# Performance work log

Hardware: AMD Instinct MI355X
Metric: run time of the kernel (lower is better)

Reference implementation:

```python
import jax, jax.numpy as jnp
import numpy as np

B, S, D, H = 2, 2048, 2048, 16
DH = D // H  # 128 head dim
ROPE_THETA = 10000.0
LN_EPS = 1e-5


def setup_inputs() -> dict:
    key = jax.random.key(0)
    k1, k2, k3 = jax.random.split(key, 3)
    positions = jnp.broadcast_to(jnp.arange(S, dtype=jnp.int64), (B, S))
    hidden_states = jax.random.normal(k1, (B, S, D), dtype=jnp.float32)
    w_qkv = jax.random.normal(k2, (D, 3 * D), dtype=jnp.float32) * 0.02
    w_out = jax.random.normal(k3, (D, D), dtype=jnp.float32) * 0.02
    return {"positions": positions, "hidden_states": hidden_states,
            "w_qkv": w_qkv, "w_out": w_out}


def _rope(x, positions):
    # NeoX-style rotary (vLLM get_rope default): rotate split halves.
    # x: [B, S, H, DH], positions: [B, S]
    half = DH // 2
    inv_freq = 1.0 / (ROPE_THETA ** (jnp.arange(0, half, dtype=jnp.float32) / half))
    ang = positions.astype(jnp.float32)[..., None] * inv_freq  # [B, S, half]
    cos = jnp.cos(ang)[:, :, None, :]  # [B, S, 1, half]
    sin = jnp.sin(ang)[:, :, None, :]
    x1, x2 = x[..., :half], x[..., half:]
    return jnp.concatenate([x1 * cos - x2 * sin, x2 * cos + x1 * sin], axis=-1)


def reference(positions, hidden_states, w_qkv, w_out):
    # LayerNorm with no affine params (elementwise_affine=False)
    mu = jnp.mean(hidden_states, axis=-1, keepdims=True)
    var = jnp.mean(jnp.square(hidden_states - mu), axis=-1, keepdims=True)
    x = (hidden_states - mu) * jax.lax.rsqrt(var + LN_EPS)

    qkv = jnp.einsum('bsd,de->bse', x, w_qkv)  # [B, S, 3D]
    q, k, v = jnp.split(qkv, 3, axis=-1)
    q = q.reshape(B, S, H, DH)
    k = k.reshape(B, S, H, DH)
    v = v.reshape(B, S, H, DH)

    q = _rope(q, positions)
    k = _rope(k, positions)

    scale = DH ** -0.5
    scores = jnp.einsum('bqhd,bkhd->bhqk', q, k) * scale  # [B, H, S, S]
    causal = jnp.tril(jnp.ones((S, S), dtype=bool))
    scores = jnp.where(causal, scores, jnp.finfo(scores.dtype).min)
    probs = jax.nn.softmax(scores, axis=-1)
    attn = jnp.einsum('bhqk,bkhd->bqhd', probs, v).reshape(B, S, D)

    return jnp.einsum('bsd,de->bse', attn, w_out)
```

## Files before the change

### kernel.cpp

```cpp
#include <hip/hip_runtime.h>


typedef __bf16 bf16x8 __attribute__((ext_vector_type(8)));
typedef float f32x4 __attribute__((ext_vector_type(4)));
typedef unsigned short u16x8 __attribute__((ext_vector_type(8)));

__device__ __forceinline__ unsigned short f2bf(float f) {
  unsigned u = __builtin_bit_cast(unsigned, f);
  u = u + 0x7fffu + ((u >> 16) & 1u);
  return (unsigned short)(u >> 16);
}

#define GLD_LDS16(gp, lp)                                                      \
  __builtin_amdgcn_global_load_lds((__attribute__((address_space(1))) void*)(gp), \
                                   (__attribute__((address_space(3))) void*)(lp), \
                                   16, 0, 0)

__global__ __launch_bounds__(256) void prep_kernel(const float* __restrict__ hs,
                                                   const float* __restrict__ wqkv,
                                                   const float* __restrict__ wout,
                                                   unsigned short* __restrict__ xb,
                                                   unsigned short* __restrict__ wqkvT,
                                                   unsigned short* __restrict__ woutT) {
  const int tid = threadIdx.x;
  int bx = blockIdx.x;
  if (bx < 4096) {
    const float* rp = hs + (size_t)bx * 2048;
    const float4 v0 = ((const float4*)rp)[tid];
    const float4 v1 = ((const float4*)rp)[tid + 256];
    float s  = v0.x + v0.y + v0.z + v0.w + v1.x + v1.y + v1.z + v1.w;
    float ss = v0.x*v0.x + v0.y*v0.y + v0.z*v0.z + v0.w*v0.w
             + v1.x*v1.x + v1.y*v1.y + v1.z*v1.z + v1.w*v1.w;
#pragma unroll
    for (int m = 1; m < 64; m <<= 1) { s += __shfl_xor(s, m); ss += __shfl_xor(ss, m); }
    __shared__ float rs[4], rss[4];
    if ((tid & 63) == 0) { rs[tid >> 6] = s; rss[tid >> 6] = ss; }
    __syncthreads();
    s  = rs[0] + rs[1] + rs[2] + rs[3];
    ss = rss[0] + rss[1] + rss[2] + rss[3];
    const float mean = s * (1.0f / 2048.0f);
    const float var  = ss * (1.0f / 2048.0f) - mean * mean;
    const float inv  = rsqrtf(var + 1e-5f);
    ushort4 o0, o1;
    o0.x = f2bf((v0.x - mean) * inv); o0.y = f2bf((v0.y - mean) * inv);
    o0.z = f2bf((v0.z - mean) * inv); o0.w = f2bf((v0.w - mean) * inv);
    o1.x = f2bf((v1.x - mean) * inv); o1.y = f2bf((v1.y - mean) * inv);
    o1.z = f2bf((v1.z - mean) * inv); o1.w = f2bf((v1.w - mean) * inv);
    ushort4* op = (ushort4*)(xb + (size_t)bx * 2048);
    op[tid] = o0; op[tid + 256] = o1;
    return;
  }
  bx -= 4096;
  const float* in;
  unsigned short* out;
  int N, nt, kt;
  if (bx < 3072) { in = wqkv; out = wqkvT; N = 6144; nt = bx % 96; kt = bx / 96; }
  else { bx -= 3072; in = wout; out = woutT; N = 2048; nt = bx & 31; kt = bx >> 5; }
  const int n0 = nt * 64, k0 = kt * 64;
  __shared__ float t[64 * 65];
  const int tx4 = (tid & 15) * 4, ty = tid >> 4;
#pragma unroll
  for (int i = 0; i < 4; i++) {
    const int k = ty + i * 16;
    const float4 v = *(const float4*)&in[(size_t)(k0 + k) * N + n0 + tx4];
    t[(tx4 + 0) * 65 + k] = v.x;
    t[(tx4 + 1) * 65 + k] = v.y;
    t[(tx4 + 2) * 65 + k] = v.z;
    t[(tx4 + 3) * 65 + k] = v.w;
  }
  __syncthreads();
  const int kc = (tid & 7) * 8, nr = tid >> 3;
#pragma unroll
  for (int i = 0; i < 2; i++) {
    const int n = nr + i * 32;
    u16x8 o;
#pragma unroll
    for (int j = 0; j < 8; j++) o[j] = f2bf(t[n * 65 + kc + j]);
    *(u16x8*)&out[(size_t)(n0 + n) * 2048 + k0 + kc] = o;
  }
}

template <int OUT_BF16, int K>
__global__ __launch_bounds__(256) void gemm_bt(const unsigned short* __restrict__ A,
                                               const unsigned short* __restrict__ Bt,
                                               void* __restrict__ Cv,
                                               int M, int N) {
  __shared__ alignas(16) unsigned short sA[128 * 64];
  __shared__ alignas(16) unsigned short sB[128 * 64];
  const int tid = threadIdx.x;
  const int lane = tid & 63, wave = tid >> 6;
  const int wm = wave >> 1, wn = wave & 1;
  const int ln15 = lane & 15, quad = lane >> 4;
  const size_t m0 = (size_t)blockIdx.y * 128, n0 = (size_t)blockIdx.x * 128;
  const unsigned short* Ag = A + m0 * (size_t)K;
  const unsigned short* Bg = Bt + n0 * (size_t)K;
  const int lr8 = lane >> 3;
  const int sc8 = ((lane & 7) ^ (lr8 & 7)) * 8;
  const int xk = ln15 & 7;

  const unsigned short* pA[4];
  const unsigned short* pB[4];
#pragma unroll
  for (int i = 0; i < 4; i++) {
    const int row = (wave * 4 + i) * 8 + lr8;
    pA[i] = Ag + (size_t)row * K + sc8;
    pB[i] = Bg + (size_t)row * K + sc8;
  }

  f32x4 acc[4][4];
#pragma unroll
  for (int mi = 0; mi < 4; mi++)
#pragma unroll
    for (int ni = 0; ni < 4; ni++) acc[mi][ni] = (f32x4){0.f, 0.f, 0.f, 0.f};

#define K_STEP(U)                                                              \
  {                                                                            \
    __syncthreads();                                                           \
    _Pragma("unroll") for (int i = 0; i < 4; i++) {                            \
      GLD_LDS16(pA[i] + (U) * 64, &sA[(wave * 4 + i) * 512]);                  \
      GLD_LDS16(pB[i] + (U) * 64, &sB[(wave * 4 + i) * 512]);                  \
    }                                                                          \
    __syncthreads();                                                           \
    _Pragma("unroll") for (int ks = 0; ks < 2; ks++) {                         \
      bf16x8 af[4], bf[4];                                                     \
      _Pragma("unroll") for (int mi = 0; mi < 4; mi++)                         \
        af[mi] = *(const bf16x8*)&sA[(wm * 64 + mi * 16 + ln15) * 64 +         \
                                     ((ks * 4 + quad) ^ xk) * 8];              \
      _Pragma("unroll") for (int ni = 0; ni < 4; ni++)                         \
        bf[ni] = *(const bf16x8*)&sB[(wn * 64 + ni * 16 + ln15) * 64 +         \
                                     ((ks * 4 + quad) ^ xk) * 8];              \
      _Pragma("unroll") for (int mi = 0; mi < 4; mi++)                         \
        _Pragma("unroll") for (int ni = 0; ni < 4; ni++)                       \
          acc[mi][ni] = __builtin_amdgcn_mfma_f32_16x16x32_bf16(               \
              af[mi], bf[ni], acc[mi][ni], 0, 0, 0);                           \
    }                                                                          \
  }

#pragma unroll 1
  for (int kt4 = 0; kt4 < K / 256; ++kt4) {
    K_STEP(0) K_STEP(1) K_STEP(2) K_STEP(3)
#pragma unroll
    for (int i = 0; i < 4; i++) { pA[i] += 256; pB[i] += 256; }
  }
#undef K_STEP

#pragma unroll
  for (int mi = 0; mi < 4; mi++)
#pragma unroll
    for (int ni = 0; ni < 4; ni++) {
      const size_t col = n0 + wn * 64 + ni * 16 + ln15;
#pragma unroll
      for (int r = 0; r < 4; r++) {
        const size_t row = m0 + wm * 64 + mi * 16 + quad * 4 + r;
        if (OUT_BF16)
          ((unsigned short*)Cv)[row * N + col] = f2bf(acc[mi][ni][r]);
        else
          ((float*)Cv)[row * N + col] = acc[mi][ni][r];
      }
    }
}

__global__ __launch_bounds__(256) void rv_kernel(const unsigned short* __restrict__ qkv,
                                                 unsigned short* __restrict__ Qo,
                                                 unsigned short* __restrict__ Ko,
                                                 unsigned short* __restrict__ VT) {
  const int tid = threadIdx.x;
  const int bx = blockIdx.x;
  if (bx < 2048) {
    const int t = bx * 256 + tid;
    const int g = t & 7;
    const int h = (t >> 3) & 15;
    const int row = t >> 7;
    const int s = row & 2047;
    const size_t base = (size_t)row * 6144 + h * 128 + g * 8;
    const bf16x8 q1 = *(const bf16x8*)&qkv[base];
    const bf16x8 q2 = *(const bf16x8*)&qkv[base + 64];
    const bf16x8 k1 = *(const bf16x8*)&qkv[base + 2048];
    const bf16x8 k2 = *(const bf16x8*)&qkv[base + 2048 + 64];
    const float qscale = 0.08838834764831845f;
    bf16x8 oq1, oq2, ok1, ok2;
#pragma unroll
    for (int j = 0; j < 8; j++) {
      const int i = g * 8 + j;
      const float freq = exp2f(-(float)i * (13.287712379549449f / 64.0f));
      float rev = (float)s * freq * 0.15915494309189535f;
      rev -= floorf(rev);
      const float ar = rev * 6.283185307179586f;
      const float sn = __sinf(ar), cs = __cosf(ar);
      const float a1 = (float)q1[j], a2 = (float)q2[j];
      const float b1 = (float)k1[j], b2 = (float)k2[j];
      oq1[j] = (__bf16)((a1 * cs - a2 * sn) * qscale);
      oq2[j] = (__bf16)((a2 * cs + a1 * sn) * qscale);
      ok1[j] = (__bf16)(b1 * cs - b2 * sn);
      ok2[j] = (__bf16)(b2 * cs + b1 * sn);
    }
    const size_t ob = ((size_t)(((row >> 11) << 4) + h) * 2048 + s) * 128 + g * 8;
    *(bf16x8*)&Qo[ob]      = oq1;
    *(bf16x8*)&Qo[ob + 64] = oq2;
    *(bf16x8*)&Ko[ob]      = ok1;
    *(bf16x8*)&Ko[ob + 64] = ok2;
    return;
  }
  const int idx = bx - 2048;
  const int s0 = (idx & 31) * 64;
  const int d0 = ((idx >> 5) & 1) * 64;
  const int bh = idx >> 6, b = bh >> 4, h = bh & 15;
  __shared__ unsigned short t[64 * 65];
  const int tx8 = (tid & 7) * 8, ty = tid >> 3;
#pragma unroll
  for (int i = 0; i < 2; i++) {
    const int s = ty + i * 32;
    const u16x8 v = *(const u16x8*)&qkv[(size_t)(b * 2048 + s0 + s) * 6144 +
                                        4096 + h * 128 + d0 + tx8];
#pragma unroll
    for (int j = 0; j < 8; j++) t[(tx8 + j) * 65 + s] = v[j];
  }
  __syncthreads();
  const int sc8 = (tid & 7) * 8, dr = tid >> 3;
#pragma unroll
  for (int i = 0; i < 2; i++) {
    const int d = dr + i * 32;
    u16x8 o;
#pragma unroll
    for (int j = 0; j < 8; j++) o[j] = t[d * 65 + sc8 + j];
    *(u16x8*)&VT[((size_t)bh * 128 + d0 + d) * 2048 + s0 + sc8] = o;
  }
}

__global__ __launch_bounds__(256) void flash_kernel(const unsigned short* __restrict__ Q,
                                                    const unsigned short* __restrict__ Kbuf,
                                                    const unsigned short* __restrict__ VT,
                                                    unsigned short* __restrict__ attn) {
  __shared__ alignas(16) unsigned short sK[2][64 * 128];
  __shared__ alignas(16) unsigned short sVT[2][128 * 64];
  __shared__ alignas(16) unsigned short sP[64 * 72];

  const int bh = blockIdx.y;
  const int b = bh >> 4, h = bh & 15;
  const int tid = threadIdx.x;
  const int lane = tid & 63, w = tid >> 6;
  const int ln15 = lane & 15, quad = lane >> 4;

  const unsigned short* Qg = Q + (size_t)bh * 2048 * 128;
  const unsigned short* Kg = Kbuf + (size_t)bh * 2048 * 128;
  const unsigned short* Vg = VT + (size_t)bh * 128 * 2048;

  const float L2E = 1.44269504088896f;
  bf16x8 onesf;
#pragma unroll
  for (int j = 0; j < 8; j++) onesf[j] = (__bf16)1.0f;

  const int kcrow = (lane >> 4);
  const int kch = (lane & 15);
  const int vcrow = (lane >> 3);
  const int vch = (lane & 7);
  const unsigned short* pK0[4];
  const unsigned short* pV0[4];
#pragma unroll
  for (int i = 0; i < 4; i++) {
    const int c = w * 4 + i;
    const int rowK = c * 4 + kcrow;
    pK0[i] = Kg + (size_t)rowK * 128 + (kch ^ (rowK & 15)) * 8;
    const int rowV = c * 8 + vcrow;
    pV0[i] = Vg + (size_t)rowV * 2048 + (vch ^ (rowV & 7)) * 8;
  }

#pragma unroll 1
  for (int t = 0; t < 2; t++) {
    const int qt = t ? (31 - (int)blockIdx.x) : (int)blockIdx.x;
    const int q0 = qt * 64;

    bf16x8 qf[4];
#pragma unroll
    for (int ks = 0; ks < 4; ks++)
      qf[ks] = *(const bf16x8*)&Qg[(size_t)(q0 + w * 16 + ln15) * 128 + ks * 32 + quad * 8];

    f32x4 o[8], ol;
#pragma unroll
    for (int nd = 0; nd < 8; nd++) o[nd] = (f32x4){0.f, 0.f, 0.f, 0.f};
    ol = (f32x4){0.f, 0.f, 0.f, 0.f};
    float mrow[4];
#pragma unroll
    for (int r = 0; r < 4; r++) mrow[r] = -1e30f;

    __syncthreads();
#pragma unroll
    for (int i = 0; i < 4; i++) GLD_LDS16(pK0[i], &sK[0][(w * 4 + i) * 512]);
#pragma unroll
    for (int i = 0; i < 4; i++) GLD_LDS16(pV0[i], &sVT[0][(w * 4 + i) * 512]);

    const unsigned short* pKn[4];
    const unsigned short* pVn[4];
#pragma unroll
    for (int i = 0; i < 4; i++) { pKn[i] = pK0[i] + 8192; pVn[i] = pV0[i] + 64; }

#pragma unroll 1
    for (int j = 0; j <= qt; j++) {
      const int cur = j & 1;
      __syncthreads();
      if (j < qt) {
        const int nxt = cur ^ 1;
#pragma unroll
        for (int i = 0; i < 4; i++) GLD_LDS16(pKn[i], &sK[nxt][(w * 4 + i) * 512]);
#pragma unroll
        for (int i = 0; i < 4; i++) GLD_LDS16(pVn[i], &sVT[nxt][(w * 4 + i) * 512]);
      }
#pragma unroll
      for (int i = 0; i < 4; i++) { pKn[i] += 8192; pVn[i] += 64; }

      f32x4 sc[4];
#pragma unroll
      for (int ni = 0; ni < 4; ni++) sc[ni] = (f32x4){0.f, 0.f, 0.f, 0.f};
      __builtin_amdgcn_s_setprio(1);
#pragma unroll
      for (int ks = 0; ks < 4; ks++) {
        bf16x8 bk[4];
#pragma unroll
        for (int ni = 0; ni < 4; ni++) {
          const int row = ni * 16 + ln15;
          const int ch = (ks * 4 + quad) ^ (row & 15);
          bk[ni] = *(const bf16x8*)&sK[cur][row * 128 + ch * 8];
        }
#pragma unroll
        for (int ni = 0; ni < 4; ni++)
          sc[ni] = __builtin_amdgcn_mfma_f32_16x16x32_bf16(qf[ks], bk[ni], sc[ni], 0, 0, 0);
      }
      __builtin_amdgcn_s_setprio(0);

      float mt[4] = {-1e30f, -1e30f, -1e30f, -1e30f};
      if (j == qt) {
        const int k0 = j * 64;
#pragma unroll
        for (int ni = 0; ni < 4; ni++) {
          const int key = k0 + ni * 16 + ln15;
#pragma unroll
          for (int r = 0; r < 4; r++) {
            const int qrow = q0 + w * 16 + quad * 4 + r;
            float v = sc[ni][r];
            if (key > qrow) v = -1e30f;
            sc[ni][r] = v;
            mt[r] = fmaxf(mt[r], v);
          }
        }
      } else {
#pragma unroll
        for (int ni = 0; ni < 4; ni++)
#pragma unroll
          for (int r = 0; r < 4; r++) mt[r] = fmaxf(mt[r], sc[ni][r]);
      }
      float m4[4];
#pragma unroll
      for (int r = 0; r < 4; r++) {
        float m = mt[r];
        m = fmaxf(m, __shfl_xor(m, 1));
        m = fmaxf(m, __shfl_xor(m, 2));
        m = fmaxf(m, __shfl_xor(m, 4));
        m = fmaxf(m, __shfl_xor(m, 8));
        m4[r] = m;
      }
      const bool defer = (m4[0] <= mrow[0] + 8.0f) & (m4[1] <= mrow[1] + 8.0f) &
                         (m4[2] <= mrow[2] + 8.0f) & (m4[3] <= mrow[3] + 8.0f);
      if (!__all(defer)) {
#pragma unroll
        for (int r = 0; r < 4; r++) {
          const float mnew = fmaxf(mrow[r], m4[r]);
          const float alpha = exp2f((mrow[r] - mnew) * L2E);
          mrow[r] = mnew;
          ol[r] *= alpha;
#pragma unroll
          for (int nd = 0; nd < 8; nd++) o[nd][r] *= alpha;
        }
      }
#pragma unroll
      for (int r = 0; r < 4; r++)
#pragma unroll
        for (int ni = 0; ni < 4; ni++)
          sc[ni][r] = exp2f((sc[ni][r] - mrow[r]) * L2E);

#pragma unroll
      for (int ni = 0; ni < 4; ni++)
#pragma unroll
        for (int r = 0; r < 4; r++)
          sP[(w * 16 + quad * 4 + r) * 72 + ni * 16 + ln15] = f2bf(sc[ni][r]);

      bf16x8 pf[2];
#pragma unroll
      for (int kk = 0; kk < 2; kk++)
        pf[kk] = *(const bf16x8*)&sP[(w * 16 + ln15) * 72 + kk * 32 + quad * 8];
      __builtin_amdgcn_s_setprio(1);
#pragma unroll
      for (int kk = 0; kk < 2; kk++) {
#pragma unroll
        for (int nd = 0; nd < 8; nd++) {
          const int row = nd * 16 + ln15;
          const int ch = (kk * 4 + quad) ^ (row & 7);
          const bf16x8 bv = *(const bf16x8*)&sVT[cur][row * 64 + ch * 8];
          o[nd] = __builtin_amdgcn_mfma_f32_16x16x32_bf16(pf[kk], bv, o[nd], 0, 0, 0);
        }
        ol = __builtin_amdgcn_mfma_f32_16x16x32_bf16(pf[kk], onesf, ol, 0, 0, 0);
      }
      __builtin_amdgcn_s_setprio(0);
    }

#pragma unroll
    for (int r = 0; r < 4; r++) {
      const float inv = 1.0f / ol[r];
      const int qrow = q0 + w * 16 + quad * 4 + r;
#pragma unroll
      for (int nd = 0; nd < 8; nd++) {
        const int d = nd * 16 + ln15;
        attn[((size_t)(b * 2048 + qrow)) * 2048 + h * 128 + d] = f2bf(o[nd][r] * inv);
      }
    }
  }
}

extern "C" void kernel_launch(void* const* d_in, const int* in_sizes, int n_in,
                              void* d_out, int out_size, void* d_ws, size_t ws_size,
                              hipStream_t stream) {
  const float* hs   = (const float*)d_in[1];
  const float* wqkv = (const float*)d_in[2];
  const float* wout = (const float*)d_in[3];
  float* out = (float*)d_out;
  char* ws = (char*)d_ws;

  unsigned short* x_bf  = (unsigned short*)(ws);
  unsigned short* wqkvT = (unsigned short*)(ws + 16777216);
  unsigned short* woutT = (unsigned short*)(ws + 41943040);
  unsigned short* qkv   = (unsigned short*)(ws + 50331648);
  unsigned short* Qb    = (unsigned short*)(ws + 100663296);
  unsigned short* Kb    = (unsigned short*)(ws + 117440512);
  unsigned short* VT    = wqkvT;
  unsigned short* attn  = x_bf;

  prep_kernel<<<4096 + 4096, 256, 0, stream>>>(hs, wqkv, wout, x_bf, wqkvT, woutT);
  gemm_bt<1, 2048><<<dim3(48, 32), 256, 0, stream>>>(x_bf, wqkvT, (void*)qkv, 4096, 6144);
  rv_kernel<<<2048 + 2048, 256, 0, stream>>>(qkv, Qb, Kb, VT);
  flash_kernel<<<dim3(16, 32), 256, 0, stream>>>(Qb, Kb, VT, attn);
  gemm_bt<0, 2048><<<dim3(16, 32), 256, 0, stream>>>(attn, woutT, (void*)out, 4096, 2048);
}
```

Measured before the change: 379.3 us.

## Fuse V transpose into QKV GEMM epilogue and double flash query tile

The QKV GEMM epilogue now writes the V columns directly in transposed per-head layout, so the separate transpose blocks in the rope kernel go away. The Q/K output buffer is narrowed to a 4096-wide stride. The flash kernel moves to 512 threads covering 128 query rows per block, with 8 waves sharing each K/V tile load and half as many blocks. Risks are fewer blocks for load balance, more LDS per block, and uncoalesced 8-byte strided stores in the V epilogue.

```diff
diff --git a/kernel.cpp b/kernel.cpp
--- a/kernel.cpp
+++ b/kernel.cpp
@@ -80,10 +80,11 @@
   }
 }
 
-template <int OUT_BF16, int K>
+template <int MODE, int K>
 __global__ __launch_bounds__(256) void gemm_bt(const unsigned short* __restrict__ A,
                                                const unsigned short* __restrict__ Bt,
                                                void* __restrict__ Cv,
+                                               unsigned short* __restrict__ VTout,
                                                int M, int N) {
   __shared__ alignas(16) unsigned short sA[128 * 64];
   __shared__ alignas(16) unsigned short sB[128 * 64];
@@ -144,6 +145,24 @@
   }
 #undef K_STEP
 
+  if (MODE == 1 && n0 >= 4096) {
+    const int b16 = (int)(m0 >> 11) * 16;
+#pragma unroll
+    for (int mi = 0; mi < 4; mi++) {
+      const int s0 = (int)(m0 & 2047) + wm * 64 + mi * 16 + quad * 4;
+#pragma unroll
+      for (int ni = 0; ni < 4; ni++) {
+        const int vcol = (int)n0 - 4096 + wn * 64 + ni * 16 + ln15;
+        const int bh = b16 + (vcol >> 7);
+        const int d = vcol & 127;
+        ushort4 o;
+        o.x = f2bf(acc[mi][ni][0]); o.y = f2bf(acc[mi][ni][1]);
+        o.z = f2bf(acc[mi][ni][2]); o.w = f2bf(acc[mi][ni][3]);
+        *(ushort4*)&VTout[((size_t)bh * 128 + d) * 2048 + s0] = o;
+      }
+    }
+    return;
+  }
 #pragma unroll
   for (int mi = 0; mi < 4; mi++)
 #pragma unroll
@@ -152,8 +171,8 @@
 #pragma unroll
       for (int r = 0; r < 4; r++) {
         const size_t row = m0 + wm * 64 + mi * 16 + quad * 4 + r;
-        if (OUT_BF16)
-          ((unsigned short*)Cv)[row * N + col] = f2bf(acc[mi][ni][r]);
+        if (MODE == 1)
+          ((unsigned short*)Cv)[row * 4096 + col] = f2bf(acc[mi][ni][r]);
         else
           ((float*)Cv)[row * N + col] = acc[mi][ni][r];
       }
@@ -162,81 +181,53 @@
 
 __global__ __launch_bounds__(256) void rv_kernel(const unsigned short* __restrict__ qkv,
                                                  unsigned short* __restrict__ Qo,
-                                                 unsigned short* __restrict__ Ko,
-                                                 unsigned short* __restrict__ VT) {
+                                                 unsigned short* __restrict__ Ko) {
   const int tid = threadIdx.x;
   const int bx = blockIdx.x;
-  if (bx < 2048) {
-    const int t = bx * 256 + tid;
-    const int g = t & 7;
-    const int h = (t >> 3) & 15;
-    const int row = t >> 7;
-    const int s = row & 2047;
-    const size_t base = (size_t)row * 6144 + h * 128 + g * 8;
-    const bf16x8 q1 = *(const bf16x8*)&qkv[base];
-    const bf16x8 q2 = *(const bf16x8*)&qkv[base + 64];
-    const bf16x8 k1 = *(const bf16x8*)&qkv[base + 2048];
-    const bf16x8 k2 = *(const bf16x8*)&qkv[base + 2048 + 64];
-    const float qscale = 0.08838834764831845f;
-    bf16x8 oq1, oq2, ok1, ok2;
-#pragma unroll
-    for (int j = 0; j < 8; j++) {
-      const int i = g * 8 + j;
-      const float freq = exp2f(-(float)i * (13.287712379549449f / 64.0f));
-      float rev = (float)s * freq * 0.15915494309189535f;
-      rev -= floorf(rev);
-      const float ar = rev * 6.283185307179586f;
-      const float sn = __sinf(ar), cs = __cosf(ar);
-      const float a1 = (float)q1[j], a2 = (float)q2[j];
-      const float b1 = (float)k1[j], b2 = (float)k2[j];
-      oq1[j] = (__bf16)((a1 * cs - a2 * sn) * qscale);
-      oq2[j] = (__bf16)((a2 * cs + a1 * sn) * qscale);
-      ok1[j] = (__bf16)(b1 * cs - b2 * sn);
-      ok2[j] = (__bf16)(b2 * cs + b1 * sn);
-    }
-    const size_t ob = ((size_t)(((row >> 11) << 4) + h) * 2048 + s) * 128 + g * 8;
-    *(bf16x8*)&Qo[ob]      = oq1;
-    *(bf16x8*)&Qo[ob + 64] = oq2;
-    *(bf16x8*)&Ko[ob]      = ok1;
-    *(bf16x8*)&Ko[ob + 64] = ok2;
-    return;
-  }
-  const int idx = bx - 2048;
-  const int s0 = (idx & 31) * 64;
-  const int d0 = ((idx >> 5) & 1) * 64;
-  const int bh = idx >> 6, b = bh >> 4, h = bh & 15;
-  __shared__ unsigned short t[64 * 65];
-  const int tx8 = (tid & 7) * 8, ty = tid >> 3;
-#pragma unroll
-  for (int i = 0; i < 2; i++) {
-    const int s = ty + i * 32;
-    const u16x8 v = *(const u16x8*)&qkv[(size_t)(b * 2048 + s0 + s) * 6144 +
-                                        4096 + h * 128 + d0 + tx8];
-#pragma unroll
-    for (int j = 0; j < 8; j++) t[(tx8 + j) * 65 + s] = v[j];
-  }
-  __syncthreads();
-  const int sc8 = (tid & 7) * 8, dr = tid >> 3;
-#pragma unroll
-  for (int i = 0; i < 2; i++) {
-    const int d = dr + i * 32;
-    u16x8 o;
-#pragma unroll
-    for (int j = 0; j < 8; j++) o[j] = t[d * 65 + sc8 + j];
-    *(u16x8*)&VT[((size_t)bh * 128 + d0 + d) * 2048 + s0 + sc8] = o;
-  }
-}
-
-__global__ __launch_bounds__(256) void flash_kernel(const unsigned short* __restrict__ Q,
+  const int t = bx * 256 + tid;
+  const int g = t & 7;
+  const int h = (t >> 3) & 15;
+  const int row = t >> 7;
+  const int s = row & 2047;
+  const size_t base = (size_t)row * 4096 + h * 128 + g * 8;
+  const bf16x8 q1 = *(const bf16x8*)&qkv[base];
+  const bf16x8 q2 = *(const bf16x8*)&qkv[base + 64];
+  const bf16x8 k1 = *(const bf16x8*)&qkv[base + 2048];
+  const bf16x8 k2 = *(const bf16x8*)&qkv[base + 2048 + 64];
+  const float qscale = 0.08838834764831845f;
+  bf16x8 oq1, oq2, ok1, ok2;
+#pragma unroll
+  for (int j = 0; j < 8; j++) {
+    const int i = g * 8 + j;
+    const float freq = exp2f(-(float)i * (13.287712379549449f / 64.0f));
+    float rev = (float)s * freq * 0.15915494309189535f;
+    rev -= floorf(rev);
+    const float ar = rev * 6.283185307179586f;
+    const float sn = __sinf(ar), cs = __cosf(ar);
+    const float a1 = (float)q1[j], a2 = (float)q2[j];
+    const float b1 = (float)k1[j], b2 = (float)k2[j];
+    oq1[j] = (__bf16)((a1 * cs - a2 * sn) * qscale);
+    oq2[j] = (__bf16)((a2 * cs + a1 * sn) * qscale);
+    ok1[j] = (__bf16)(b1 * cs - b2 * sn);
+    ok2[j] = (__bf16)(b2 * cs + b1 * sn);
+  }
+  const size_t ob = ((size_t)(((row >> 11) << 4) + h) * 2048 + s) * 128 + g * 8;
+  *(bf16x8*)&Qo[ob]      = oq1;
+  *(bf16x8*)&Qo[ob + 64] = oq2;
+  *(bf16x8*)&Ko[ob]      = ok1;
+  *(bf16x8*)&Ko[ob + 64] = ok2;
+}
+
+__global__ __launch_bounds__(512) void flash_kernel(const unsigned short* __restrict__ Q,
                                                     const unsigned short* __restrict__ Kbuf,
                                                     const unsigned short* __restrict__ VT,
                                                     unsigned short* __restrict__ attn) {
   __shared__ alignas(16) unsigned short sK[2][64 * 128];
   __shared__ alignas(16) unsigned short sVT[2][128 * 64];
-  __shared__ alignas(16) unsigned short sP[64 * 72];
+  __shared__ alignas(16) unsigned short sP[128 * 72];
 
   const int bh = blockIdx.y;
-  const int b = bh >> 4, h = bh & 15;
+  const int b = bh >> 4;
   const int tid = threadIdx.x;
   const int lane = tid & 63, w = tid >> 6;
   const int ln15 = lane & 15, quad = lane >> 4;
@@ -254,11 +245,11 @@
   const int kch = (lane & 15);
   const int vcrow = (lane >> 3);
   const int vch = (lane & 7);
-  const unsigned short* pK0[4];
-  const unsigned short* pV0[4];
-#pragma unroll
-  for (int i = 0; i < 4; i++) {
-    const int c = w * 4 + i;
+  const unsigned short* pK0[2];
+  const unsigned short* pV0[2];
+#pragma unroll
+  for (int i = 0; i < 2; i++) {
+    const int c = w * 2 + i;
     const int rowK = c * 4 + kcrow;
     pK0[i] = Kg + (size_t)rowK * 128 + (kch ^ (rowK & 15)) * 8;
     const int rowV = c * 8 + vcrow;
@@ -267,8 +258,9 @@
 
 #pragma unroll 1
   for (int t = 0; t < 2; t++) {
-    const int qt = t ? (31 - (int)blockIdx.x) : (int)blockIdx.x;
-    const int q0 = qt * 64;
+    const int qt = t ? (15 - (int)blockIdx.x) : (int)blockIdx.x;
+    const int q0 = qt * 128;
+    const int jmax = 2 * qt + 1;
 
     bf16x8 qf[4];
 #pragma unroll
@@ -285,28 +277,28 @@
 
     __syncthreads();
 #pragma unroll
-    for (int i = 0; i < 4; i++) GLD_LDS16(pK0[i], &sK[0][(w * 4 + i) * 512]);
-#pragma unroll
-    for (int i = 0; i < 4; i++) GLD_LDS16(pV0[i], &sVT[0][(w * 4 + i) * 512]);
-
-    const unsigned short* pKn[4];
-    const unsigned short* pVn[4];
-#pragma unroll
-    for (int i = 0; i < 4; i++) { pKn[i] = pK0[i] + 8192; pVn[i] = pV0[i] + 64; }
+    for (int i = 0; i < 2; i++) GLD_LDS16(pK0[i], &sK[0][(w * 2 + i) * 512]);
+#pragma unroll
+    for (int i = 0; i < 2; i++) GLD_LDS16(pV0[i], &sVT[0][(w * 2 + i) * 512]);
+
+    const unsigned short* pKn[2];
+    const unsigned short* pVn[2];
+#pragma unroll
+    for (int i = 0; i < 2; i++) { pKn[i] = pK0[i] + 8192; pVn[i] = pV0[i] + 64; }
 
 #pragma unroll 1
-    for (int j = 0; j <= qt; j++) {
+    for (int j = 0; j <= jmax; j++) {
       const int cur = j & 1;
       __syncthreads();
-      if (j < qt) {
+      if (j < jmax) {
         const int nxt = cur ^ 1;
 #pragma unroll
-        for (int i = 0; i < 4; i++) GLD_LDS16(pKn[i], &sK[nxt][(w * 4 + i) * 512]);
-#pragma unroll
-        for (int i = 0; i < 4; i++) GLD_LDS16(pVn[i], &sVT[nxt][(w * 4 + i) * 512]);
-      }
-#pragma unroll
-      for (int i = 0; i < 4; i++) { pKn[i] += 8192; pVn[i] += 64; }
+        for (int i = 0; i < 2; i++) GLD_LDS16(pKn[i], &sK[nxt][(w * 2 + i) * 512]);
+#pragma unroll
+        for (int i = 0; i < 2; i++) GLD_LDS16(pVn[i], &sVT[nxt][(w * 2 + i) * 512]);
+      }
+#pragma unroll
+      for (int i = 0; i < 2; i++) { pKn[i] += 8192; pVn[i] += 64; }
 
       f32x4 sc[4];
 #pragma unroll
@@ -328,7 +320,7 @@
       __builtin_amdgcn_s_setprio(0);
 
       float mt[4] = {-1e30f, -1e30f, -1e30f, -1e30f};
-      if (j == qt) {
+      if (j >= 2 * qt) {
         const int k0 = j * 64;
 #pragma unroll
         for (int ni = 0; ni < 4; ni++) {
@@ -402,6 +394,7 @@
       __builtin_amdgcn_s_setprio(0);
     }
 
+    const int h = bh & 15;
 #pragma unroll
     for (int r = 0; r < 4; r++) {
       const float inv = 1.0f / ol[r];
@@ -424,18 +417,18 @@
   float* out = (float*)d_out;
   char* ws = (char*)d_ws;
 
-  unsigned short* x_bf  = (unsigned short*)(ws);
-  unsigned short* wqkvT = (unsigned short*)(ws + 16777216);
-  unsigned short* woutT = (unsigned short*)(ws + 41943040);
-  unsigned short* qkv   = (unsigned short*)(ws + 50331648);
-  unsigned short* Qb    = (unsigned short*)(ws + 100663296);
-  unsigned short* Kb    = (unsigned short*)(ws + 117440512);
-  unsigned short* VT    = wqkvT;
-  unsigned short* attn  = x_bf;
+  unsigned short* x_bf   = (unsigned short*)(ws);
+  unsigned short* wqkvT  = (unsigned short*)(ws + 16777216);
+  unsigned short* woutT  = (unsigned short*)(ws + 41943040);
+  unsigned short* qkvQK  = (unsigned short*)(ws + 50331648);
+  unsigned short* VTbuf  = (unsigned short*)(ws + 83886080);
+  unsigned short* Qb     = (unsigned short*)(ws + 100663296);
+  unsigned short* Kb     = (unsigned short*)(ws + 117440512);
+  unsigned short* attn   = x_bf;
 
   prep_kernel<<<4096 + 4096, 256, 0, stream>>>(hs, wqkv, wout, x_bf, wqkvT, woutT);
-  gemm_bt<1, 2048><<<dim3(48, 32), 256, 0, stream>>>(x_bf, wqkvT, (void*)qkv, 4096, 6144);
-  rv_kernel<<<2048 + 2048, 256, 0, stream>>>(qkv, Qb, Kb, VT);
-  flash_kernel<<<dim3(16, 32), 256, 0, stream>>>(Qb, Kb, VT, attn);
-  gemm_bt<0, 2048><<<dim3(16, 32), 256, 0, stream>>>(attn, woutT, (void*)out, 4096, 2048);
-}
+  gemm_bt<1, 2048><<<dim3(48, 32), 256, 0, stream>>>(x_bf, wqkvT, (void*)qkvQK, VTbuf, 4096, 6144);
+  rv_kernel<<<2048, 256, 0, stream>>>(qkvQK, Qb, Kb);
+  flash_kernel<<<dim3(8, 32), 512, 0, stream>>>(Qb, Kb, VTbuf, attn);
+  gemm_bt<0, 2048><<<dim3(16, 32), 256, 0, stream>>>(attn, woutT, (void*)out, nullptr, 4096, 2048);
+}
```

After: 385.9 us. Within noise of the previous version (+1.7%).
